# Optimization experiments

Hardware: AMD Instinct MI355X
Metric: run time of the kernel (lower is better)

## Reference

```python
import jax, jax.numpy as jnp
from jax import lax
import numpy as np

B, H, W = 1, 128, 256
C = 32           # feature_channels
D = 32           # max_disp
HID = 64         # hidden_channels in message passing
ITERS = 5


def conv2d(x, w, b):
    # x: [N, Cin, H, W], w: [Cout, Cin, kh, kw], SAME padding, stride 1
    y = lax.conv_general_dilated(x, w, (1, 1), [(1, 1), (1, 1)],
                                 dimension_numbers=('NCHW', 'OIHW', 'NCHW'))
    return y + b[None, :, None, None]


def setup_inputs() -> dict:
    key = jax.random.key(0)
    ks = jax.random.split(key, 12)
    def p(k, shape, s=0.05):
        return jax.random.normal(k, shape, jnp.float32) * s
    return {
        'left_img':  jax.random.normal(ks[0], (B, 3, H, W), jnp.float32),
        'right_img': jax.random.normal(ks[1], (B, 3, H, W), jnp.float32),
        # feature extractor (3 -> C -> C)
        'fe_w1': p(ks[2], (C, 3, 3, 3)),  'fe_b1': jnp.zeros((C,), jnp.float32),
        'fe_w2': p(ks[3], (C, C, 3, 3)),  'fe_b2': jnp.zeros((C,), jnp.float32),
        # cost volume 1x1 conv over concat(left, shifted_right): 2C -> 1
        'cv_w': p(ks[4], (2 * C,)),       'cv_b': jnp.zeros((), jnp.float32),
        # message passing: concat(feature, belief)=C+1 -> HID -> 1
        'mp_w1': p(ks[5], (HID, C + 1, 3, 3)), 'mp_b1': jnp.zeros((HID,), jnp.float32),
        'mp_w2': p(ks[6], (1, HID, 3, 3)),     'mp_b2': jnp.zeros((1,), jnp.float32),
        # refinement: concat(left_img, disparity)=4 -> 32 -> 32 -> 1 residual
        'rf_w1': p(ks[7], (32, 4, 3, 3)),  'rf_b1': jnp.zeros((32,), jnp.float32),
        'rf_w2': p(ks[8], (32, 32, 3, 3)), 'rf_b2': jnp.zeros((32,), jnp.float32),
        'rf_w3': p(ks[9], (1, 32, 3, 3)),  'rf_b3': jnp.zeros((1,), jnp.float32),
    }


def _forward(left_img, right_img, fe_w1, fe_b1, fe_w2, fe_b2, cv_w, cv_b,
             mp_w1, mp_b1, mp_w2, mp_b2, rf_w1, rf_b1, rf_w2, rf_b2, rf_w3, rf_b3):
    def feat(img):
        h = jax.nn.relu(conv2d(img, fe_w1, fe_b1))
        return jax.nn.relu(conv2d(h, fe_w2, fe_b2))

    lf = feat(left_img)    # [B, C, H, W]
    rf = feat(right_img)   # [B, C, H, W]

    # Cost volume: shift right features by each disparity, 1x1 conv on concat.
    rf_sh = jnp.stack([jnp.pad(rf, ((0, 0), (0, 0), (0, 0), (d, 0)))[..., :W]
                       for d in range(D)])                     # [D, B, C, H, W]
    pair = jnp.concatenate([jnp.broadcast_to(lf[None], rf_sh.shape), rf_sh], axis=2)  # [D,B,2C,H,W]
    cost = jnp.einsum('dbchw,c->dbhw', pair, cv_w) + cv_b      # [D, B, H, W]
    data = cost[:, :, None]                                     # [D, B, 1, H, W]

    # Iterative BP message passing, vectorized across all disparity planes.
    def mp(data_term):  # data_term: [B, 1, H, W]
        def step(belief, _):
            x = jnp.concatenate([lf, belief], axis=1)           # [B, C+1, H, W]
            hdn = jax.nn.relu(conv2d(x, mp_w1, mp_b1))          # [B, HID, H, W]
            msg = conv2d(hdn, mp_w2, mp_b2)                     # [B, 1, H, W]
            return data_term + msg, None
        belief, _ = lax.scan(step, data_term, None, length=ITERS)
        return belief

    beliefs = jax.vmap(mp)(data)                                # [D, B, 1, H, W]
    refined = jnp.transpose(beliefs, (1, 2, 0, 3, 4))           # [B, 1, D, H, W]

    prob = jax.nn.softmax(-refined, axis=2)                     # [B, 1, D, H, W]
    idx = jnp.arange(D, dtype=prob.dtype)
    disparity = jnp.einsum('bodhw,d->bohw', prob, idx)          # [B, 1, H, W]

    # Refinement network (residual).
    x = jnp.concatenate([left_img, disparity], axis=1)          # [B, 4, H, W]
    r = jax.nn.relu(conv2d(x, rf_w1, rf_b1))
    r = jax.nn.relu(conv2d(r, rf_w2, rf_b2))
    res = conv2d(r, rf_w3, rf_b3)
    return disparity + res                                      # [B, 1, H, W]


def reference(left_img, right_img, fe_w1, fe_b1, fe_w2, fe_b2, cv_w, cv_b,
              mp_w1, mp_b1, mp_w2, mp_b2, rf_w1, rf_b1, rf_w2, rf_b2, rf_w3, rf_b3):
    return _forward(left_img, right_img, fe_w1, fe_b1, fe_w2, fe_b2, cv_w, cv_b,
                    mp_w1, mp_b1, mp_w2, mp_b2, rf_w1, rf_b1, rf_w2, rf_b2, rf_w3, rf_b3)
```

## Files before the change

kernel.cpp:

```cpp
#include <hip/hip_runtime.h>
#include <hip/hip_bf16.h>

#define H 128
#define W 256
#define HW (H*W)
#define NC 32
#define ND 32
#define NHID 64

__global__ __launch_bounds__(256) void conv3x3(
        const float* __restrict__ in0, const float* __restrict__ in1,
        float* __restrict__ out0, float* __restrict__ out1,
        const float* __restrict__ w, const float* __restrict__ b,
        int CIN, int COUT, int wstride, int dorelu,
        const float* __restrict__ addin) {
    __shared__ float wS[2304];
    __shared__ float tile[2][4][10][35];
    const int tid = threadIdx.x;
    const int zg = (COUT + 7) >> 3;
    const int img = blockIdx.z / zg;
    const int cog = blockIdx.z % zg;
    const float* in = img ? in1 : in0;
    float* out = img ? out1 : out0;
    const int cobase = cog * 8;
    int nco = COUT - cobase; if (nco > 8) nco = 8;
    const int gx0 = blockIdx.x * 32, gy0 = blockIdx.y * 8;
    const int tx = tid & 31, ty = tid >> 5;

    const int wcnt = nco * CIN * 9;
    for (int i = tid; i < wcnt; i += 256) {
        int co = i / (CIN * 9), rem = i % (CIN * 9);
        wS[i] = w[(size_t)(cobase + co) * wstride + rem];
    }

    const int nst = (CIN + 3) >> 2;
    {
        int nch = CIN < 4 ? CIN : 4;
        for (int i = tid; i < nch * 340; i += 256) {
            int ch = i / 340, rem = i % 340;
            int r = rem / 34, cc = rem % 34;
            int gy = gy0 + r - 1, gx = gx0 + cc - 1;
            tile[0][ch][r][cc] = (gy >= 0 && gy < H && gx >= 0 && gx < W)
                                 ? in[(size_t)ch * HW + gy * W + gx] : 0.f;
        }
    }
    __syncthreads();

    float acc[8];
#pragma unroll
    for (int i = 0; i < 8; i++) acc[i] = 0.f;

    for (int s = 0; s < nst; s++) {
        const int c0 = s * 4;
        int nch = CIN - c0; if (nch > 4) nch = 4;
        if (s + 1 < nst) {
            const int c1 = c0 + 4;
            int nch2 = CIN - c1; if (nch2 > 4) nch2 = 4;
            const int nb = (s + 1) & 1;
            for (int i = tid; i < nch2 * 340; i += 256) {
                int ch = i / 340, rem = i % 340;
                int r = rem / 34, cc = rem % 34;
                int gy = gy0 + r - 1, gx = gx0 + cc - 1;
                tile[nb][ch][r][cc] = (gy >= 0 && gy < H && gx >= 0 && gx < W)
                                      ? in[(size_t)(c1 + ch) * HW + gy * W + gx] : 0.f;
            }
        }
        const int cb = s & 1;
        for (int ch = 0; ch < nch; ch++) {
            float v[9];
#pragma unroll
            for (int ky = 0; ky < 3; ky++)
#pragma unroll
                for (int kx = 0; kx < 3; kx++)
                    v[ky * 3 + kx] = tile[cb][ch][ty + ky][tx + kx];
            const int wb = (c0 + ch) * 9;
#pragma unroll
            for (int co = 0; co < 8; co++) {
                if (co < nco) {
                    const float* wp = &wS[co * CIN * 9 + wb];
#pragma unroll
                    for (int k = 0; k < 9; k++) acc[co] += wp[k] * v[k];
                }
            }
        }
        __syncthreads();
    }

    const int gy = gy0 + ty, gx = gx0 + tx;
    const float ad = addin ? addin[gy * W + gx] : 0.f;
#pragma unroll
    for (int co = 0; co < 8; co++) {
        if (co < nco) {
            float r = acc[co] + b[cobase + co];
            if (dorelu) r = fmaxf(r, 0.f);
            r += ad;
            out[(size_t)(cobase + co) * HW + gy * W + gx] = r;
        }
    }
}

__global__ void chan_dot(const float* __restrict__ lf, const float* __restrict__ rf,
                         const float* __restrict__ cvw,
                         float* __restrict__ lsum, float* __restrict__ rsum) {
    int p = blockIdx.x * 256 + threadIdx.x;
    if (p >= HW) return;
    float ls = 0.f, rs = 0.f;
    for (int c = 0; c < NC; c++) {
        ls += lf[c * HW + p] * cvw[c];
        rs += rf[c * HW + p] * cvw[NC + c];
    }
    lsum[p] = ls;
    rsum[p] = rs;
}

__global__ void cost_expand(const float* __restrict__ lsum, const float* __restrict__ rsum,
                            const float* __restrict__ cvb,
                            float* __restrict__ cost, float* __restrict__ bel) {
    int idx = blockIdx.x * 256 + threadIdx.x;
    if (idx >= ND * HW) return;
    int d = idx / HW, p = idx % HW;
    int col = p & (W - 1);
    float c = lsum[p] + cvb[0];
    if (col >= d) c += rsum[p - d];
    cost[idx] = c;
    bel[idx] = c;
}

__global__ void a_transpose(const float* __restrict__ A, float* __restrict__ At) {
    __shared__ float t[64][65];
    int p0 = blockIdx.x * 64;
    int tx = threadIdx.x & 63;
    int ty = threadIdx.x >> 6;
#pragma unroll
    for (int r = 0; r < 16; r++) {
        int hid = ty * 16 + r;
        t[tx][hid] = A[(size_t)hid * HW + p0 + tx];
    }
    __syncthreads();
#pragma unroll
    for (int r = 0; r < 16; r++) {
        int p = ty * 16 + r;
        At[(size_t)(p0 + p) * 64 + tx] = t[p][tx];
    }
}

#define LOADROW(YC, AR)                                                        \
  {                                                                            \
    if ((YC) >= 0 && (YC) < H) {                                               \
      AR[0] = bp[e0off];                                                       \
      _Pragma("unroll") for (int j = 1; j < 17; j++) AR[j] = bp[(j - 8) * 64]; \
      AR[17] = bp[e17off];                                                     \
    }                                                                          \
    bp += W * 64;                                                              \
  }

#define COMPUTE(U, AR, HARR)                                                   \
  {                                                                            \
    const int yc_ = y0 + (U);                                                  \
    if (yc_ < 0 || yc_ >= H) {                                                 \
      _Pragma("unroll") for (int j = 0; j < 18; j++) HARR[j] = 0.f;            \
    } else {                                                                   \
      float bw_[3][3];                                                         \
      _Pragma("unroll") for (int r = 0; r < 3; r++) {                          \
        bw_[r][0] = belW[(U) + 1 + r][0];                                      \
        bw_[r][1] = belW[(U) + 1 + r][1];                                      \
      }                                                                        \
      _Pragma("unroll") for (int j = 0; j < 18; j++) {                         \
        float acc_ = AR[j];                                                    \
        _Pragma("unroll") for (int r = 0; r < 3; r++)                          \
          bw_[r][(j + 2) % 3] = belW[(U) + 1 + r][j + 2];                      \
        _Pragma("unroll") for (int r = 0; r < 3; r++)                          \
          _Pragma("unroll") for (int c = 0; c < 3; c++)                        \
            acc_ += w1[r * 3 + c] * bw_[r][(j + c) % 3];                       \
        HARR[j] = fmaxf(acc_, 0.f);                                            \
      }                                                                        \
      if (x0 == 0) HARR[0] = 0.f;                                              \
      if (x0 == W - 16) HARR[17] = 0.f;                                        \
    }                                                                          \
  }

#define EMIT3(T, HH2, HH1, HH0)                                                \
  {                                                                            \
    _Pragma("unroll") for (int jo = 0; jo < 16; jo++) {                        \
      float pp = w2[0] * HH2[jo] + w2[1] * HH2[jo + 1] + w2[2] * HH2[jo + 2]   \
               + w2[3] * HH1[jo] + w2[4] * HH1[jo + 1] + w2[5] * HH1[jo + 2]   \
               + w2[6] * HH0[jo] + w2[7] * HH0[jo + 1] + w2[8] * HH0[jo + 2];  \
      partW[jo][lane] = pp;                                                    \
    }                                                                          \
    asm volatile("s_waitcnt lgkmcnt(0)" ::: "memory");                         \
    {                                                                          \
      const float4* pr = (const float4*)&partW[pq][qq * 16];                   \
      float4 v0 = pr[0], v1 = pr[1], v2 = pr[2], v3 = pr[3];                   \
      float s_ = (((v0.x + v0.y) + (v0.z + v0.w)) +                            \
                  ((v1.x + v1.y) + (v1.z + v1.w))) +                           \
                 (((v2.x + v2.y) + (v2.z + v2.w)) +                            \
                  ((v3.x + v3.y) + (v3.z + v3.w)));                            \
      s_ += __shfl_xor(s_, 16);                                                \
      s_ += __shfl_xor(s_, 32);                                                \
      if (qq == 0)                                                             \
        bout[obase + (size_t)(T) * W] = costW[(T)][pq] + s_ + b2;              \
      asm volatile("s_waitcnt lgkmcnt(0)" ::: "memory");                       \
    }                                                                          \
  }

#define STEP(T, AIN, AOUT, HX2, HX1, HX0, DOLOAD)                              \
  {                                                                            \
    if (DOLOAD) { LOADROW(y0 + (T) + 2, AOUT); }                               \
    COMPUTE((T) + 1, AIN, HX0);                                                \
    EMIT3(T, HX2, HX1, HX0);                                                   \
  }

__global__ __launch_bounds__(256, 1) void mp_iter_fast(
    const float* __restrict__ At,
    const float* __restrict__ cost,
    const float* __restrict__ bin,
    float* __restrict__ bout,
    const float* __restrict__ mp_w1,
    const float* __restrict__ mp_w2,
    const float* __restrict__ mp_b2) {
    __shared__ float belS[4][12][20];
    __shared__ float costS[4][8][16];
    __shared__ float partS[4][16][68];

    const int tid = threadIdx.x;
    const int lane = tid & 63;
    const int lw = tid >> 6;
    float (*belW)[20]  = belS[lw];
    float (*costW)[16] = costS[lw];
    float (*partW)[68] = partS[lw];

    const int i = blockIdx.x;
    const int xcd = i & 7;
    const int jj = i >> 3;
    const int ybl = jj & 1;
    const int sl = (jj >> 1) & 15;
    const int d4 = jj >> 5;
    const int d = d4 * 4 + lw;
    const int x0 = sl * 16;
    const int y0 = (xcd + 8 * ybl) * 8;

    float w1[9], w2[9];
#pragma unroll
    for (int k = 0; k < 9; k++) {
        w1[k] = mp_w1[lane * 297 + 288 + k];
        w2[k] = mp_w2[lane * 9 + k];
    }
    const float b2 = mp_b2[0];

    const float* bp = At + (size_t)(y0 - 1) * (W * 64) + (x0 + 7) * 64 + lane;
    const int e0off  = (x0 == 0)      ? -448 : -512;
    const int e17off = (x0 == W - 16) ?  512 :  576;

    const float* beld = bin + (size_t)d * HW;
#pragma unroll
    for (int it = 0; it < 4; it++) {
        int idx = it * 64 + lane;
        if (idx < 240) {
            int r = idx / 20, c = idx % 20;
            int gy = y0 - 2 + r, gx = x0 - 2 + c;
            belW[r][c] = (gy >= 0 && gy < H && gx >= 0 && gx < W) ? beld[gy * W + gx] : 0.f;
        }
    }
#pragma unroll
    for (int it = 0; it < 2; it++) {
        int idx = it * 64 + lane;
        int r = idx >> 4, c = idx & 15;
        costW[r][c] = cost[(size_t)d * HW + (size_t)(y0 + r) * W + x0 + c];
    }
    asm volatile("s_waitcnt lgkmcnt(0)" ::: "memory");

    const int pq = lane & 15, qq = lane >> 4;
    const size_t obase = (size_t)d * HW + (size_t)y0 * W + x0 + pq;

    float aA[18], aB[18];
    float hA[18], hB[18], hC[18];

    LOADROW(y0 - 1, aA);
    LOADROW(y0, aB);
    COMPUTE(-1, aA, hA);
    LOADROW(y0 + 1, aA);
    COMPUTE(0, aB, hB);

    STEP(0, aA, aB, hA, hB, hC, 1)
    STEP(1, aB, aA, hB, hC, hA, 1)
    STEP(2, aA, aB, hC, hA, hB, 1)
    STEP(3, aB, aA, hA, hB, hC, 1)
    STEP(4, aA, aB, hB, hC, hA, 1)
    STEP(5, aB, aA, hC, hA, hB, 1)
    STEP(6, aA, aB, hA, hB, hC, 1)
    STEP(7, aB, aA, hB, hC, hA, 0)
}

__global__ void softmax_disp(const float* __restrict__ bel, const float* __restrict__ left,
                             float* __restrict__ disp, float* __restrict__ x4) {
    int p = blockIdx.x * 256 + threadIdx.x;
    if (p >= HW) return;
    float v[ND];
    float m = -1e30f;
#pragma unroll
    for (int d = 0; d < ND; d++) {
        v[d] = -bel[d * HW + p];
        m = fmaxf(m, v[d]);
    }
    float s = 0.f, ws = 0.f;
#pragma unroll
    for (int d = 0; d < ND; d++) {
        float e = __expf(v[d] - m);
        s += e;
        ws += e * (float)d;
    }
    float dv = ws / s;
    disp[p] = dv;
    x4[3 * HW + p] = dv;
    x4[p] = left[p];
    x4[HW + p] = left[HW + p];
    x4[2 * HW + p] = left[2 * HW + p];
}

extern "C" void kernel_launch(void* const* d_in, const int* in_sizes, int n_in,
                              void* d_out, int out_size, void* d_ws, size_t ws_size,
                              hipStream_t stream) {
    const float* left   = (const float*)d_in[0];
    const float* right  = (const float*)d_in[1];
    const float* fe_w1  = (const float*)d_in[2];
    const float* fe_b1  = (const float*)d_in[3];
    const float* fe_w2  = (const float*)d_in[4];
    const float* fe_b2  = (const float*)d_in[5];
    const float* cv_w   = (const float*)d_in[6];
    const float* cv_b   = (const float*)d_in[7];
    const float* mp_w1  = (const float*)d_in[8];
    const float* mp_b1  = (const float*)d_in[9];
    const float* mp_w2  = (const float*)d_in[10];
    const float* mp_b2  = (const float*)d_in[11];
    const float* rf_w1  = (const float*)d_in[12];
    const float* rf_b1  = (const float*)d_in[13];
    const float* rf_w2  = (const float*)d_in[14];
    const float* rf_b2  = (const float*)d_in[15];
    const float* rf_w3  = (const float*)d_in[16];
    const float* rf_b3  = (const float*)d_in[17];
    float* out = (float*)d_out;

    float* ws = (float*)d_ws;
    float* At    = ws;
    float* tmp0  = ws;
    float* tmp1  = ws + 1048576;
    float* lf    = ws + 2097152;
    float* rfeat = ws + 3145728;
    float* cost  = ws + 4194304;
    float* Araw  = ws + 4194304;
    float* bel   = ws + 5242880;
    float* bel2  = ws + 6291456;
    float* lsum  = ws + 7340032;
    float* rsum  = ws + 7372800;
    float* disp  = ws + 7405568;
    float* x4    = ws + 7438336;

    dim3 blk(256);

    conv3x3<<<dim3(8, 16, 8), blk, 0, stream>>>(left, right, tmp0, tmp1, fe_w1, fe_b1, 3, 32, 27, 1, nullptr);
    conv3x3<<<dim3(8, 16, 8), blk, 0, stream>>>(tmp0, tmp1, lf, rfeat, fe_w2, fe_b2, 32, 32, 288, 1, nullptr);

    chan_dot<<<dim3(HW / 256), blk, 0, stream>>>(lf, rfeat, cv_w, lsum, rsum);

    conv3x3<<<dim3(8, 16, 8), blk, 0, stream>>>(lf, lf, Araw, Araw, mp_w1, mp_b1, 32, 64, 297, 0, nullptr);
    a_transpose<<<dim3(HW / 64), blk, 0, stream>>>(Araw, At);

    cost_expand<<<dim3(ND * HW / 256), blk, 0, stream>>>(lsum, rsum, cv_b, cost, bel);

    dim3 gmp(2048);
    mp_iter_fast<<<gmp, blk, 0, stream>>>(At, cost, bel,  bel2, mp_w1, mp_w2, mp_b2);
    mp_iter_fast<<<gmp, blk, 0, stream>>>(At, cost, bel2, bel,  mp_w1, mp_w2, mp_b2);
    mp_iter_fast<<<gmp, blk, 0, stream>>>(At, cost, bel,  bel2, mp_w1, mp_w2, mp_b2);
    mp_iter_fast<<<gmp, blk, 0, stream>>>(At, cost, bel2, bel,  mp_w1, mp_w2, mp_b2);
    mp_iter_fast<<<gmp, blk, 0, stream>>>(At, cost, bel,  bel2, mp_w1, mp_w2, mp_b2);

    softmax_disp<<<dim3(HW / 256), blk, 0, stream>>>(bel2, left, disp, x4);

    conv3x3<<<dim3(8, 16, 4), blk, 0, stream>>>(x4, x4, At, At, rf_w1, rf_b1, 4, 32, 36, 1, nullptr);
    conv3x3<<<dim3(8, 16, 4), blk, 0, stream>>>(At, At, rfeat, rfeat, rf_w2, rf_b2, 32, 32, 288, 1, nullptr);
    conv3x3<<<dim3(8, 16, 1), blk, 0, stream>>>(rfeat, rfeat, out, out, rf_w3, rf_b3, 32, 1, 288, 0, disp);
}
```

Before: 555.2 us.

## Stream belief rows and cost into registers instead of LDS staging in mp kernel

The message-passing kernel used to stage a 12x20 belief halo and an 8x16 cost tile in shared memory per wave, then wait on LDS before computing. Belief rows are now loaded straight from global memory into a rotating four-row register ring, with each row prefetched one step ahead, and cost values are held in per-lane registers. Two s_waitcnt fences in the reduction path are also removed. The aim is to drop the LDS round trip and its upfront stall and overlap belief loads with compute, at the cost of higher register pressure and redundant global loads, since every lane reads the same belief row. Removing the waitcnt fences relies on the compiler to order the partW LDS writes and reads correctly.

```diff
diff --git a/kernel.cpp b/kernel.cpp
--- a/kernel.cpp
+++ b/kernel.cpp
@@ -154,24 +154,32 @@
     bp += W * 64;                                                              \
   }
 
-#define COMPUTE(U, AR, HARR)                                                   \
+#define LOADBEL(Z, BR)                                                         \
+  {                                                                            \
+    const int z_ = (Z);                                                        \
+    if (z_ >= 0 && z_ < H) {                                                   \
+      const float* br_ = beld + (size_t)z_ * W + x0;                           \
+      BR[0] = xnot0 ? br_[-2] : 0.f;                                           \
+      BR[1] = xnot0 ? br_[-1] : 0.f;                                           \
+      _Pragma("unroll") for (int q = 0; q < 16; q++) BR[q + 2] = br_[q];       \
+      BR[18] = xnotE ? br_[16] : 0.f;                                          \
+      BR[19] = xnotE ? br_[17] : 0.f;                                          \
+    } else {                                                                   \
+      _Pragma("unroll") for (int q = 0; q < 20; q++) BR[q] = 0.f;              \
+    }                                                                          \
+  }
+
+#define COMPUTE(U, AR, HARR, B0, B1, B2)                                       \
   {                                                                            \
     const int yc_ = y0 + (U);                                                  \
     if (yc_ < 0 || yc_ >= H) {                                                 \
       _Pragma("unroll") for (int j = 0; j < 18; j++) HARR[j] = 0.f;            \
     } else {                                                                   \
-      float bw_[3][3];                                                         \
-      _Pragma("unroll") for (int r = 0; r < 3; r++) {                          \
-        bw_[r][0] = belW[(U) + 1 + r][0];                                      \
-        bw_[r][1] = belW[(U) + 1 + r][1];                                      \
-      }                                                                        \
       _Pragma("unroll") for (int j = 0; j < 18; j++) {                         \
         float acc_ = AR[j];                                                    \
-        _Pragma("unroll") for (int r = 0; r < 3; r++)                          \
-          bw_[r][(j + 2) % 3] = belW[(U) + 1 + r][j + 2];                      \
-        _Pragma("unroll") for (int r = 0; r < 3; r++)                          \
-          _Pragma("unroll") for (int c = 0; c < 3; c++)                        \
-            acc_ += w1[r * 3 + c] * bw_[r][(j + c) % 3];                       \
+        acc_ += w1[0] * B0[j] + w1[1] * B0[j + 1] + w1[2] * B0[j + 2];         \
+        acc_ += w1[3] * B1[j] + w1[4] * B1[j + 1] + w1[5] * B1[j + 2];         \
+        acc_ += w1[6] * B2[j] + w1[7] * B2[j + 1] + w1[8] * B2[j + 2];         \
         HARR[j] = fmaxf(acc_, 0.f);                                            \
       }                                                                        \
       if (x0 == 0) HARR[0] = 0.f;                                              \
@@ -187,7 +195,6 @@
                + w2[6] * HH0[jo] + w2[7] * HH0[jo + 1] + w2[8] * HH0[jo + 2];  \
       partW[jo][lane] = pp;                                                    \
     }                                                                          \
-    asm volatile("s_waitcnt lgkmcnt(0)" ::: "memory");                         \
     {                                                                          \
       const float4* pr = (const float4*)&partW[pq][qq * 16];                   \
       float4 v0 = pr[0], v1 = pr[1], v2 = pr[2], v3 = pr[3];                   \
@@ -197,16 +204,15 @@
                   ((v3.x + v3.y) + (v3.z + v3.w)));                            \
       s_ += __shfl_xor(s_, 16);                                                \
       s_ += __shfl_xor(s_, 32);                                                \
-      if (qq == 0)                                                             \
-        bout[obase + (size_t)(T) * W] = costW[(T)][pq] + s_ + b2;              \
-      asm volatile("s_waitcnt lgkmcnt(0)" ::: "memory");                       \
-    }                                                                          \
-  }
-
-#define STEP(T, AIN, AOUT, HX2, HX1, HX0, DOLOAD)                              \
-  {                                                                            \
+      if (qq == 0) bout[obase + (size_t)(T) * W] = cst[(T)] + s_ + b2;         \
+    }                                                                          \
+  }
+
+#define STEP(T, AIN, AOUT, HX2, HX1, HX0, B0, B1, B2, BN, DOLOAD, DOBEL)       \
+  {                                                                            \
+    if (DOBEL) { LOADBEL(y0 + (T) + 3, BN); }                                  \
     if (DOLOAD) { LOADROW(y0 + (T) + 2, AOUT); }                               \
-    COMPUTE((T) + 1, AIN, HX0);                                                \
+    COMPUTE((T) + 1, AIN, HX0, B0, B1, B2);                                    \
     EMIT3(T, HX2, HX1, HX0);                                                   \
   }
 
@@ -218,15 +224,11 @@
     const float* __restrict__ mp_w1,
     const float* __restrict__ mp_w2,
     const float* __restrict__ mp_b2) {
-    __shared__ float belS[4][12][20];
-    __shared__ float costS[4][8][16];
     __shared__ float partS[4][16][68];
 
     const int tid = threadIdx.x;
     const int lane = tid & 63;
-    const int lw = tid >> 6;
-    float (*belW)[20]  = belS[lw];
-    float (*costW)[16] = costS[lw];
+    const int lw = __builtin_amdgcn_readfirstlane(tid >> 6);
     float (*partW)[68] = partS[lw];
 
     const int i = blockIdx.x;
@@ -238,6 +240,7 @@
     const int d = d4 * 4 + lw;
     const int x0 = sl * 16;
     const int y0 = (xcd + 8 * ybl) * 8;
+    const bool xnot0 = (x0 > 0), xnotE = (x0 < W - 16);
 
     float w1[9], w2[9];
 #pragma unroll
@@ -252,43 +255,36 @@
     const int e17off = (x0 == W - 16) ?  512 :  576;
 
     const float* beld = bin + (size_t)d * HW;
-#pragma unroll
-    for (int it = 0; it < 4; it++) {
-        int idx = it * 64 + lane;
-        if (idx < 240) {
-            int r = idx / 20, c = idx % 20;
-            int gy = y0 - 2 + r, gx = x0 - 2 + c;
-            belW[r][c] = (gy >= 0 && gy < H && gx >= 0 && gx < W) ? beld[gy * W + gx] : 0.f;
-        }
-    }
-#pragma unroll
-    for (int it = 0; it < 2; it++) {
-        int idx = it * 64 + lane;
-        int r = idx >> 4, c = idx & 15;
-        costW[r][c] = cost[(size_t)d * HW + (size_t)(y0 + r) * W + x0 + c];
-    }
-    asm volatile("s_waitcnt lgkmcnt(0)" ::: "memory");
-
     const int pq = lane & 15, qq = lane >> 4;
     const size_t obase = (size_t)d * HW + (size_t)y0 * W + x0 + pq;
 
+    float cst[8];
+#pragma unroll
+    for (int t = 0; t < 8; t++) cst[t] = cost[obase + (size_t)t * W];
+
     float aA[18], aB[18];
     float hA[18], hB[18], hC[18];
-
+    float bl0[20], bl1[20], bl2[20], bl3[20];
+
+    LOADBEL(y0 - 2, bl0);
+    LOADBEL(y0 - 1, bl1);
+    LOADBEL(y0,     bl2);
     LOADROW(y0 - 1, aA);
-    LOADROW(y0, aB);
-    COMPUTE(-1, aA, hA);
+    LOADROW(y0,     aB);
+    COMPUTE(-1, aA, hA, bl0, bl1, bl2);
+    LOADBEL(y0 + 1, bl3);
     LOADROW(y0 + 1, aA);
-    COMPUTE(0, aB, hB);
-
-    STEP(0, aA, aB, hA, hB, hC, 1)
-    STEP(1, aB, aA, hB, hC, hA, 1)
-    STEP(2, aA, aB, hC, hA, hB, 1)
-    STEP(3, aB, aA, hA, hB, hC, 1)
-    STEP(4, aA, aB, hB, hC, hA, 1)
-    STEP(5, aB, aA, hC, hA, hB, 1)
-    STEP(6, aA, aB, hA, hB, hC, 1)
-    STEP(7, aB, aA, hB, hC, hA, 0)
+    COMPUTE(0, aB, hB, bl1, bl2, bl3);
+    LOADBEL(y0 + 2, bl0);
+
+    STEP(0, aA, aB, hA, hB, hC, bl2, bl3, bl0, bl1, 1, 1)
+    STEP(1, aB, aA, hB, hC, hA, bl3, bl0, bl1, bl2, 1, 1)
+    STEP(2, aA, aB, hC, hA, hB, bl0, bl1, bl2, bl3, 1, 1)
+    STEP(3, aB, aA, hA, hB, hC, bl1, bl2, bl3, bl0, 1, 1)
+    STEP(4, aA, aB, hB, hC, hA, bl2, bl3, bl0, bl1, 1, 1)
+    STEP(5, aB, aA, hC, hA, hB, bl3, bl0, bl1, bl2, 1, 1)
+    STEP(6, aA, aB, hA, hB, hC, bl0, bl1, bl2, bl3, 1, 1)
+    STEP(7, aB, aA, hB, hC, hA, bl1, bl2, bl3, bl0, 0, 0)
 }
 
 __global__ void softmax_disp(const float* __restrict__ bel, const float* __restrict__ left,
```

Result: faster. 525.9 us (-5.3%).
